# Kernel tuning notes

Measured on AMD Instinct MI355X. Metric: run time of the kernel, lower is better.

Reference implementation:

```python
import jax, jax.numpy as jnp
import numpy as np

N_NODES = 50000
N_EDGES = 800000
NEG_SLOPE = 0.2


def _edge_softmax(scores, dst, n):
    # scores: [E, H]; softmax over edges grouped by destination node
    m = jax.ops.segment_max(scores, dst, num_segments=n)          # [N, H]
    ex = jnp.exp(scores - m[dst])                                 # [E, H]
    s = jax.ops.segment_sum(ex, dst, num_segments=n)              # [N, H]
    return ex / s[dst]


def _gat_layer(h, W, attn_l, attn_r, bias, src, dst, n, heads, out_d):
    feat = (h @ W).reshape(n, heads, out_d)                       # [N, H, D]
    el = jnp.sum(feat * attn_l, axis=-1)                          # [N, H]
    er = jnp.sum(feat * attn_r, axis=-1)                          # [N, H]
    e = jax.nn.leaky_relu(el[src] + er[dst], NEG_SLOPE)           # [E, H]
    alpha = _edge_softmax(e, dst, n)                              # [E, H]
    msg = feat[src] * alpha[:, :, None]                           # [E, H, D]
    rst = jax.ops.segment_sum(msg, dst, num_segments=n)           # [N, H, D]
    return rst + bias.reshape(1, heads, out_d)


def setup_inputs() -> dict:
    key = jax.random.key(0)
    ks = jax.random.split(key, 12)
    in_dim, hid, heads, out_dim = 128, 64, 4, 64
    sc = 0.1
    return {
        "emb": jax.random.normal(ks[0], (N_NODES, in_dim), jnp.float32),
        "src": jax.random.randint(ks[1], (N_EDGES,), 0, N_NODES, jnp.int32),
        "dst": jax.random.randint(ks[2], (N_EDGES,), 0, N_NODES, jnp.int32),
        "W1": jax.random.normal(ks[3], (in_dim, heads * hid), jnp.float32) * sc,
        "attn_l1": jax.random.normal(ks[4], (1, heads, hid), jnp.float32) * sc,
        "attn_r1": jax.random.normal(ks[5], (1, heads, hid), jnp.float32) * sc,
        "b1": jax.random.normal(ks[6], (heads * hid,), jnp.float32) * sc,
        "W2": jax.random.normal(ks[7], (heads * hid, out_dim), jnp.float32) * sc,
        "attn_l2": jax.random.normal(ks[8], (1, 1, out_dim), jnp.float32) * sc,
        "attn_r2": jax.random.normal(ks[9], (1, 1, out_dim), jnp.float32) * sc,
        "b2": jax.random.normal(ks[10], (out_dim,), jnp.float32) * sc,
    }


def reference(emb, src, dst, W1, attn_l1, attn_r1, b1, W2, attn_l2, attn_r2, b2):
    n = emb.shape[0]
    h = _gat_layer(emb, W1, attn_l1, attn_r1, b1, src, dst, n, 4, 64)   # [N,4,64]
    h = jax.nn.relu(h).reshape(n, 4 * 64)                                # [N,256]
    h = _gat_layer(h, W2, attn_l2, attn_r2, b2, src, dst, n, 1, 64)      # [N,1,64]
    return h.reshape(n, 64)
```

## Files before the change

### kernel.cpp

```cpp
#include <hip/hip_runtime.h>
#include <hip/hip_bf16.h>
#include <math.h>

#define DIV_UP(a,b) (((a)+(b)-1)/(b))

typedef __attribute__((ext_vector_type(8))) short short8v;
typedef __attribute__((ext_vector_type(4))) float f32x4;

__device__ __forceinline__ float bf_lo(unsigned u){ union{unsigned x; float f;} v; v.x = u << 16; return v.f; }
__device__ __forceinline__ float bf_hi(unsigned u){ union{unsigned x; float f;} v; v.x = u & 0xffff0000u; return v.f; }
__device__ __forceinline__ unsigned short f2bf(float f){
  union{float f; unsigned u;} v; v.f = f;
  unsigned r = v.u + 0x7fff + ((v.u >> 16) & 1);
  return (unsigned short)(r >> 16);
}
__device__ __forceinline__ unsigned packbf(float a, float b){
  return (unsigned)f2bf(a) | ((unsigned)f2bf(b) << 16);
}
__device__ __forceinline__ float lrelu(float x){ return x > 0.f ? x : 0.2f*x; }

__global__ void k_count_deg(const int* __restrict__ dst, int* __restrict__ deg, int E){
  int i = blockIdx.x*blockDim.x + threadIdx.x;
  if (i < E) atomicAdd(&deg[dst[i]], 1);
}

__global__ __launch_bounds__(256) void k_scan1(const int* __restrict__ deg,
                                               int* __restrict__ blocksum, int N){
  int b = blockIdx.x;
  int base = b*1024 + threadIdx.x*4;
  int s = 0;
  if (base + 3 < N){
    int4 v = *(const int4*)&deg[base];
    s = v.x + v.y + v.z + v.w;
  } else {
    for (int i = 0; i < 4; i++){ int idx = base + i; if (idx < N) s += deg[idx]; }
  }
  #pragma unroll
  for (int o = 32; o; o >>= 1) s += __shfl_down(s, o);
  __shared__ int ws[4];
  int wid = threadIdx.x >> 6, lane = threadIdx.x & 63;
  if (lane == 0) ws[wid] = s;
  __syncthreads();
  if (threadIdx.x == 0) blocksum[b] = ws[0] + ws[1] + ws[2] + ws[3];
}

__global__ void k_scan2(int* __restrict__ blocksum, int nb){
  int lane = threadIdx.x;
  int carry = 0;
  for (int base = 0; base < nb; base += 64){
    int idx = base + lane;
    int orig = (idx < nb) ? blocksum[idx] : 0;
    int v = orig;
    #pragma unroll
    for (int o = 1; o < 64; o <<= 1){ int t = __shfl_up(v, o); if (lane >= o) v += t; }
    if (idx < nb) blocksum[idx] = carry + v - orig;
    carry += __shfl(v, 63);
  }
}

__global__ __launch_bounds__(256) void k_scan3(const int* __restrict__ deg,
                                               const int* __restrict__ blockoff,
                                               int* __restrict__ row_start,
                                               int* __restrict__ cursor, int N){
  int b = blockIdx.x;
  int base = b*1024 + threadIdx.x*4;
  int v[4];
  #pragma unroll
  for (int i = 0; i < 4; i++){ int idx = base + i; v[i] = (idx < N) ? deg[idx] : 0; }
  int s = v[0] + v[1] + v[2] + v[3];
  int lane = threadIdx.x & 63, wid = threadIdx.x >> 6;
  int inc = s;
  #pragma unroll
  for (int o = 1; o < 64; o <<= 1){ int t = __shfl_up(inc, o); if (lane >= o) inc += t; }
  __shared__ int wsum[4];
  if (lane == 63) wsum[wid] = inc;
  __syncthreads();
  int woff = 0;
  #pragma unroll
  for (int i = 0; i < 4; i++) if (i < wid) woff += wsum[i];
  int run = blockoff[b] + woff + inc - s;
  #pragma unroll
  for (int i = 0; i < 4; i++){
    int idx = base + i;
    if (idx < N){ row_start[idx] = run; cursor[idx] = run; run += v[i]; }
  }
  if (base < N && base + 4 >= N) row_start[N] = run;
}

__global__ void k_fillw4(const int* __restrict__ dst, const int* __restrict__ src,
                         int* __restrict__ cursor, int* __restrict__ srcp,
                         int* __restrict__ dstp,
                         const float4* __restrict__ el4, const float4* __restrict__ er4,
                         float4* __restrict__ w4, int E){
  int i = blockIdx.x*blockDim.x + threadIdx.x;
  if (i < E){
    int d = dst[i], s = src[i];
    int p = atomicAdd(&cursor[d], 1);
    srcp[p] = s; dstp[p] = d;
    float4 l = el4[s], r = er4[d];
    float4 w;
    w.x = __expf(lrelu(l.x + r.x));
    w.y = __expf(lrelu(l.y + r.y));
    w.z = __expf(lrelu(l.z + r.z));
    w.w = __expf(lrelu(l.w + r.w));
    w4[p] = w;
  }
}

__global__ void k_edgew1(const int* __restrict__ srcp, const int* __restrict__ dstp,
                         const float* __restrict__ el, const float* __restrict__ er,
                         float* __restrict__ w1, int E){
  int i = blockIdx.x*blockDim.x + threadIdx.x;
  if (i < E) w1[i] = __expf(lrelu(el[srcp[i]] + er[dstp[i]]));
}

template<int K, int H, bool ABF>
__global__ __launch_bounds__(256) void k_gemm_mfma(const void* __restrict__ Av,
      const float* __restrict__ B, int ldb,
      unsigned short* __restrict__ Cbf,
      const float* __restrict__ al, const float* __restrict__ ar,
      float* __restrict__ el, float* __restrict__ er, int M){
  constexpr int KP = K + 8;
  __shared__ alignas(16) __hip_bfloat16 At[64][KP];
  __shared__ alignas(16) __hip_bfloat16 Bt[64][KP];
  __shared__ float elp[2][64], erp[2][64];
  const int tid = threadIdx.x;
  const int lane = tid & 63, w = tid >> 6;
  const int mw = w >> 1, nw = w & 1;
  const int m0 = blockIdx.x * 64, by = blockIdx.y, n0 = by * 64;

  if constexpr (!ABF){
    const float* A = (const float*)Av;
    #pragma unroll
    for (int i = 0; i < K/16; i++){
      int q = tid + i*256;
      int row = q / (K/4), c4 = q % (K/4);
      float4 a = make_float4(0.f,0.f,0.f,0.f);
      if (m0 + row < M) a = *(const float4*)&A[(size_t)(m0+row)*K + c4*4];
      *(uint2*)&At[row][c4*4] = make_uint2(packbf(a.x,a.y), packbf(a.z,a.w));
    }
  } else {
    const __hip_bfloat16* A = (const __hip_bfloat16*)Av;
    #pragma unroll
    for (int i = 0; i < K/32; i++){
      int q = tid + i*256;
      int row = q / (K/8), c8 = q % (K/8);
      uint4 u = make_uint4(0,0,0,0);
      if (m0 + row < M) u = *(const uint4*)&A[(size_t)(m0+row)*K + c8*8];
      *(uint4*)&At[row][c8*8] = u;
    }
  }
  #pragma unroll
  for (int i = 0; i < K/16; i++){
    int q = tid + i*256;
    int c = q & 63, k4 = q >> 6;
    float b0 = B[(size_t)(k4*4+0)*ldb + n0 + c];
    float b1 = B[(size_t)(k4*4+1)*ldb + n0 + c];
    float b2 = B[(size_t)(k4*4+2)*ldb + n0 + c];
    float b3 = B[(size_t)(k4*4+3)*ldb + n0 + c];
    *(uint2*)&Bt[c][k4*4] = make_uint2(packbf(b0,b1), packbf(b2,b3));
  }
  __syncthreads();

  f32x4 acc[2][2];
  #pragma unroll
  for (int i = 0; i < 2; i++)
    #pragma unroll
    for (int j = 0; j < 2; j++)
      #pragma unroll
      for (int r = 0; r < 4; r++) acc[i][j][r] = 0.f;

  const int rbase = mw*32, cbase = nw*32;
  const int fr = lane & 15, fg = lane >> 4;
  #pragma unroll
  for (int ks = 0; ks < K/32; ks++){
    short8v a0 = *(const short8v*)&At[rbase + fr     ][ks*32 + fg*8];
    short8v a1 = *(const short8v*)&At[rbase + 16 + fr][ks*32 + fg*8];
    short8v b0 = *(const short8v*)&Bt[cbase + fr     ][ks*32 + fg*8];
    short8v b1 = *(const short8v*)&Bt[cbase + 16 + fr][ks*32 + fg*8];
    acc[0][0] = __builtin_amdgcn_mfma_f32_16x16x32_bf16(a0, b0, acc[0][0], 0,0,0);
    acc[0][1] = __builtin_amdgcn_mfma_f32_16x16x32_bf16(a0, b1, acc[0][1], 0,0,0);
    acc[1][0] = __builtin_amdgcn_mfma_f32_16x16x32_bf16(a1, b0, acc[1][0], 0,0,0);
    acc[1][1] = __builtin_amdgcn_mfma_f32_16x16x32_bf16(a1, b1, acc[1][1], 0,0,0);
  }

  float alv[2], arv[2];
  #pragma unroll
  for (int nt = 0; nt < 2; nt++){
    int col = cbase + nt*16 + fr;
    alv[nt] = al[by*64 + col];
    arv[nt] = ar[by*64 + col];
  }
  #pragma unroll
  for (int mt = 0; mt < 2; mt++){
    #pragma unroll
    for (int r = 0; r < 4; r++){
      float pl = acc[mt][0][r]*alv[0] + acc[mt][1][r]*alv[1];
      float pr = acc[mt][0][r]*arv[0] + acc[mt][1][r]*arv[1];
      #pragma unroll
      for (int o = 1; o < 16; o <<= 1){ pl += __shfl_xor(pl, o); pr += __shfl_xor(pr, o); }
      if (fr == 0){
        int rl = rbase + mt*16 + fg*4 + r;
        elp[nw][rl] = pl; erp[nw][rl] = pr;
      }
    }
  }
  const int NN = H*64;
  #pragma unroll
  for (int mt = 0; mt < 2; mt++){
    #pragma unroll
    for (int r = 0; r < 4; r++){
      int row = m0 + rbase + mt*16 + fg*4 + r;
      if (row < M){
        #pragma unroll
        for (int nt = 0; nt < 2; nt++)
          Cbf[(size_t)row*NN + n0 + cbase + nt*16 + fr] = f2bf(acc[mt][nt][r]);
      }
    }
  }
  __syncthreads();
  if (tid < 64){
    int row = m0 + tid;
    if (row < M){
      el[(size_t)row*H + by] = elp[0][tid] + elp[1][tid];
      er[(size_t)row*H + by] = erp[0][tid] + erp[1][tid];
    }
  }
}

__global__ __launch_bounds__(256) void k_gath4(const uint4* __restrict__ fbase,
      const float* __restrict__ w4, const int* __restrict__ row_start,
      const int* __restrict__ srcp, const float* __restrict__ bias,
      __hip_bfloat16* __restrict__ outb, int N, int nwaves){
  int wv = threadIdx.x >> 6, lane = threadIdx.x & 63;
  int g = lane >> 4, j = lane & 15, h = j >> 2;
  const unsigned jo2 = (unsigned)(j << 1);

  int n = blockIdx.x*4 + wv;
  if (n >= N) return;
  int rs = row_start[n], re = row_start[n+1];

  while (true){
    int deg = re - rs;
    int nn = n + nwaves;
    int rs_n = 0, re_n = 0;
    if (nn < N){ rs_n = row_start[nn]; re_n = row_start[nn+1]; }

    float acc[16];
    #pragma unroll
    for (int k = 0; k < 16; k++) acc[k] = 0.f;
    float Sacc = 0.f;

    int i = 0;
    int full = deg & ~15;
    for (; i < full; i += 16){
      float wb[4]; uint4 u0[4], u1[4];
      #pragma unroll
      for (int k = 0; k < 4; k++){
        unsigned e = (unsigned)(rs + i + k*4 + g);
        int sb = srcp[e];
        wb[k] = w4[(e << 2) + h];
        unsigned fi = ((unsigned)sb << 5) + jo2;
        u0[k] = fbase[fi];
        u1[k] = fbase[fi + 1];
      }
      #pragma unroll
      for (int k = 0; k < 4; k++){
        float wk = wb[k];
        Sacc += wk;
        acc[0]  += bf_lo(u0[k].x)*wk; acc[1]  += bf_hi(u0[k].x)*wk;
        acc[2]  += bf_lo(u0[k].y)*wk; acc[3]  += bf_hi(u0[k].y)*wk;
        acc[4]  += bf_lo(u0[k].z)*wk; acc[5]  += bf_hi(u0[k].z)*wk;
        acc[6]  += bf_lo(u0[k].w)*wk; acc[7]  += bf_hi(u0[k].w)*wk;
        acc[8]  += bf_lo(u1[k].x)*wk; acc[9]  += bf_hi(u1[k].x)*wk;
        acc[10] += bf_lo(u1[k].y)*wk; acc[11] += bf_hi(u1[k].y)*wk;
        acc[12] += bf_lo(u1[k].z)*wk; acc[13] += bf_hi(u1[k].z)*wk;
        acc[14] += bf_lo(u1[k].w)*wk; acc[15] += bf_hi(u1[k].w)*wk;
      }
    }
    if (i < deg){
      float wb[4]; uint4 u0[4], u1[4];
      #pragma unroll
      for (int k = 0; k < 4; k++){
        int e = i + k*4 + g;
        wb[k] = 0.f;
        u0[k] = make_uint4(0,0,0,0); u1[k] = make_uint4(0,0,0,0);
        if (e < deg){
          unsigned ee = (unsigned)(rs + e);
          int sb = srcp[ee];
          wb[k] = w4[(ee << 2) + h];
          unsigned fi = ((unsigned)sb << 5) + jo2;
          u0[k] = fbase[fi];
          u1[k] = fbase[fi + 1];
        }
      }
      #pragma unroll
      for (int k = 0; k < 4; k++){
        float wk = wb[k];
        Sacc += wk;
        acc[0]  += bf_lo(u0[k].x)*wk; acc[1]  += bf_hi(u0[k].x)*wk;
        acc[2]  += bf_lo(u0[k].y)*wk; acc[3]  += bf_hi(u0[k].y)*wk;
        acc[4]  += bf_lo(u0[k].z)*wk; acc[5]  += bf_hi(u0[k].z)*wk;
        acc[6]  += bf_lo(u0[k].w)*wk; acc[7]  += bf_hi(u0[k].w)*wk;
        acc[8]  += bf_lo(u1[k].x)*wk; acc[9]  += bf_hi(u1[k].x)*wk;
        acc[10] += bf_lo(u1[k].y)*wk; acc[11] += bf_hi(u1[k].y)*wk;
        acc[12] += bf_lo(u1[k].z)*wk; acc[13] += bf_hi(u1[k].z)*wk;
        acc[14] += bf_lo(u1[k].w)*wk; acc[15] += bf_hi(u1[k].w)*wk;
      }
    }

    #pragma unroll
    for (int k = 0; k < 16; k++){
      acc[k] += __shfl_xor(acc[k], 16);
      acc[k] += __shfl_xor(acc[k], 32);
    }
    Sacc += __shfl_xor(Sacc, 16);
    Sacc += __shfl_xor(Sacc, 32);
    if (g == 0){
      float inv = (deg > 0 && Sacc > 0.f) ? 1.f / Sacc : 0.f;
      float4 b0 = *(const float4*)&bias[j*16 + 0];
      float4 b1 = *(const float4*)&bias[j*16 + 4];
      float4 b2 = *(const float4*)&bias[j*16 + 8];
      float4 b3 = *(const float4*)&bias[j*16 + 12];
      float v[16];
      v[0]=acc[0]*inv+b0.x;  v[1]=acc[1]*inv+b0.y;  v[2]=acc[2]*inv+b0.z;  v[3]=acc[3]*inv+b0.w;
      v[4]=acc[4]*inv+b1.x;  v[5]=acc[5]*inv+b1.y;  v[6]=acc[6]*inv+b1.z;  v[7]=acc[7]*inv+b1.w;
      v[8]=acc[8]*inv+b2.x;  v[9]=acc[9]*inv+b2.y;  v[10]=acc[10]*inv+b2.z; v[11]=acc[11]*inv+b2.w;
      v[12]=acc[12]*inv+b3.x; v[13]=acc[13]*inv+b3.y; v[14]=acc[14]*inv+b3.z; v[15]=acc[15]*inv+b3.w;
      #pragma unroll
      for (int k = 0; k < 16; k++) v[k] = fmaxf(v[k], 0.f);
      uint4 o0, o1;
      o0.x = packbf(v[0], v[1]);   o0.y = packbf(v[2], v[3]);
      o0.z = packbf(v[4], v[5]);   o0.w = packbf(v[6], v[7]);
      o1.x = packbf(v[8], v[9]);   o1.y = packbf(v[10], v[11]);
      o1.z = packbf(v[12], v[13]); o1.w = packbf(v[14], v[15]);
      uint4* op = (uint4*)outb + (size_t)n*32 + (j << 1);
      op[0] = o0; op[1] = o1;
    }

    if (nn >= N) break;
    n = nn; rs = rs_n; re = re_n;
  }
}

__global__ __launch_bounds__(256) void k_gath1(const uint2* __restrict__ fbase,
      const float* __restrict__ w1, const int* __restrict__ row_start,
      const int* __restrict__ srcp, const float* __restrict__ bias,
      float* __restrict__ out, int N, int nwaves){
  int wv = threadIdx.x >> 6, lane = threadIdx.x & 63;
  int g = lane >> 4, j = lane & 15;
  const unsigned jo = (unsigned)j;

  int n = blockIdx.x*4 + wv;
  if (n >= N) return;
  int rs = row_start[n], re = row_start[n+1];

  while (true){
    int deg = re - rs;
    int nn = n + nwaves;
    int rs_n = 0, re_n = 0;
    if (nn < N){ rs_n = row_start[nn]; re_n = row_start[nn+1]; }

    float acc[4] = {0.f, 0.f, 0.f, 0.f};
    float Sacc = 0.f;

    int i = 0;
    int full = deg & ~15;
    for (; i < full; i += 16){
      float wb[4]; uint2 u[4];
      #pragma unroll
      for (int k = 0; k < 4; k++){
        unsigned e = (unsigned)(rs + i + k*4 + g);
        int sb = srcp[e];
        wb[k] = w1[e];
        u[k] = fbase[((unsigned)sb << 4) + jo];
      }
      #pragma unroll
      for (int k = 0; k < 4; k++){
        float wk = wb[k];
        Sacc += wk;
        acc[0] += bf_lo(u[k].x)*wk; acc[1] += bf_hi(u[k].x)*wk;
        acc[2] += bf_lo(u[k].y)*wk; acc[3] += bf_hi(u[k].y)*wk;
      }
    }
    if (i < deg){
      float wb[4]; uint2 u[4];
      #pragma unroll
      for (int k = 0; k < 4; k++){
        int e = i + k*4 + g;
        wb[k] = 0.f;
        u[k] = make_uint2(0,0);
        if (e < deg){
          unsigned ee = (unsigned)(rs + e);
          int sb = srcp[ee];
          wb[k] = w1[ee];
          u[k] = fbase[((unsigned)sb << 4) + jo];
        }
      }
      #pragma unroll
      for (int k = 0; k < 4; k++){
        float wk = wb[k];
        Sacc += wk;
        acc[0] += bf_lo(u[k].x)*wk; acc[1] += bf_hi(u[k].x)*wk;
        acc[2] += bf_lo(u[k].y)*wk; acc[3] += bf_hi(u[k].y)*wk;
      }
    }

    #pragma unroll
    for (int k = 0; k < 4; k++){
      acc[k] += __shfl_xor(acc[k], 16);
      acc[k] += __shfl_xor(acc[k], 32);
    }
    Sacc += __shfl_xor(Sacc, 16);
    Sacc += __shfl_xor(Sacc, 32);
    if (g == 0){
      float inv = (deg > 0 && Sacc > 0.f) ? 1.f / Sacc : 0.f;
      float4 b = *(const float4*)&bias[j*4];
      float4 o;
      o.x = acc[0]*inv + b.x; o.y = acc[1]*inv + b.y;
      o.z = acc[2]*inv + b.z; o.w = acc[3]*inv + b.w;
      *(float4*)&out[(size_t)n*64 + j*4] = o;
    }

    if (nn >= N) break;
    n = nn; rs = rs_n; re = re_n;
  }
}

extern "C" void kernel_launch(void* const* d_in, const int* in_sizes, int n_in,
                              void* d_out, int out_size, void* d_ws, size_t ws_size,
                              hipStream_t stream) {
  const float* emb = (const float*)d_in[0];
  const int*   src = (const int*)d_in[1];
  const int*   dst = (const int*)d_in[2];
  const float* W1  = (const float*)d_in[3];
  const float* al1 = (const float*)d_in[4];
  const float* ar1 = (const float*)d_in[5];
  const float* b1  = (const float*)d_in[6];
  const float* W2  = (const float*)d_in[7];
  const float* al2 = (const float*)d_in[8];
  const float* ar2 = (const float*)d_in[9];
  const float* b2  = (const float*)d_in[10];
  float* out = (float*)d_out;

  const int N = in_sizes[0] / 128;
  const int E = in_sizes[1];

  char* p = (char*)d_ws;
  auto alloc = [&](size_t bytes) -> void* {
    void* r = (void*)p; p += (bytes + 255) & ~(size_t)255; return r;
  };
  __hip_bfloat16* feat1b = (__hip_bfloat16*)alloc((size_t)N*256*2);
  __hip_bfloat16* h1b    = (__hip_bfloat16*)alloc((size_t)N*256*2);
  __hip_bfloat16* feat2b = (__hip_bfloat16*)alloc((size_t)N*64*2);
  float* el1             = (float*)alloc((size_t)N*4*4);
  float* er1             = (float*)alloc((size_t)N*4*4);
  float* el2             = (float*)alloc((size_t)N*4);
  float* er2             = (float*)alloc((size_t)N*4);
  int*   deg             = (int*)alloc((size_t)N*4);
  int*   row_start       = (int*)alloc((size_t)(N+1)*4);
  int*   cursor          = (int*)alloc((size_t)N*4);
  int*   blocksum        = (int*)alloc((size_t)DIV_UP(N,1024)*4);
  int*   srcp            = (int*)alloc((size_t)E*4);
  int*   dstp            = (int*)alloc((size_t)E*4);
  float* w4              = (float*)alloc((size_t)E*16);
  float* w1              = w4;

  const int nb = DIV_UP(N, 1024);
  const int gblocks = min(DIV_UP(N, 4), 2048);
  const int nwaves  = gblocks * 4;

  hipMemsetAsync(deg, 0, (size_t)N*4, stream);
  k_count_deg<<<DIV_UP(E,256), 256, 0, stream>>>(dst, deg, E);
  k_scan1<<<nb, 256, 0, stream>>>(deg, blocksum, N);
  k_scan2<<<1, 64, 0, stream>>>(blocksum, nb);
  k_scan3<<<nb, 256, 0, stream>>>(deg, blocksum, row_start, cursor, N);

  k_gemm_mfma<128,4,false><<<dim3(DIV_UP(N,64), 4), 256, 0, stream>>>(
      emb, W1, 256, (unsigned short*)feat1b, al1, ar1, el1, er1, N);
  k_fillw4<<<DIV_UP(E,256), 256, 0, stream>>>(dst, src, cursor, srcp, dstp,
      (const float4*)el1, (const float4*)er1, (float4*)w4, E);
  k_gath4<<<gblocks, 256, 0, stream>>>((const uint4*)feat1b, w4, row_start,
                                       srcp, b1, h1b, N, nwaves);
  k_gemm_mfma<256,1,true><<<dim3(DIV_UP(N,64), 1), 256, 0, stream>>>(
      h1b, W2, 64, (unsigned short*)feat2b, al2, ar2, el2, er2, N);
  k_edgew1<<<DIV_UP(E,256), 256, 0, stream>>>(srcp, dstp, el2, er2, w1, E);
  k_gath1<<<gblocks, 256, 0, stream>>>((const uint2*)feat2b, w1, row_start,
                                       srcp, b2, out, N, nwaves);
}
```

Measured before the change: 235.4 us.

## Fold block-offset scan into scan3 and loop GEMM1 over heads per block

Removes the single-wave k_scan2 launch: each scan3 block now computes its own block offset by summing the preceding block sums inside one wave. The layer-1 GEMM becomes a dedicated kernel where each block loads and converts its 64-row A tile to bf16 once and loops over all four 64-column head tiles, instead of a 2D grid that reloads A per head. This cuts one launch and the repeated A traffic and bf16 conversion, at the cost of fewer blocks and serialized B-tile loads inside each block.

Measured after the change: 229.3 us. -2.6%, faster.

```diff
diff --git a/kernel.cpp b/kernel.cpp
--- a/kernel.cpp
+++ b/kernel.cpp
@@ -44,25 +44,22 @@
   if (threadIdx.x == 0) blocksum[b] = ws[0] + ws[1] + ws[2] + ws[3];
 }
 
-__global__ void k_scan2(int* __restrict__ blocksum, int nb){
-  int lane = threadIdx.x;
-  int carry = 0;
-  for (int base = 0; base < nb; base += 64){
-    int idx = base + lane;
-    int orig = (idx < nb) ? blocksum[idx] : 0;
-    int v = orig;
-    #pragma unroll
-    for (int o = 1; o < 64; o <<= 1){ int t = __shfl_up(v, o); if (lane >= o) v += t; }
-    if (idx < nb) blocksum[idx] = carry + v - orig;
-    carry += __shfl(v, 63);
-  }
-}
-
 __global__ __launch_bounds__(256) void k_scan3(const int* __restrict__ deg,
-                                               const int* __restrict__ blockoff,
+                                               const int* __restrict__ blocksum, int nb,
                                                int* __restrict__ row_start,
                                                int* __restrict__ cursor, int N){
   int b = blockIdx.x;
+  __shared__ int s_boff;
+  if (threadIdx.x < 64){
+    int acc = 0;
+    for (int base = 0; base < nb; base += 64){
+      int idx = base + threadIdx.x;
+      if (idx < nb && idx < b) acc += blocksum[idx];
+    }
+    #pragma unroll
+    for (int o = 32; o; o >>= 1) acc += __shfl_down(acc, o);
+    if (threadIdx.x == 0) s_boff = acc;
+  }
   int base = b*1024 + threadIdx.x*4;
   int v[4];
   #pragma unroll
@@ -78,7 +75,7 @@
   int woff = 0;
   #pragma unroll
   for (int i = 0; i < 4; i++) if (i < wid) woff += wsum[i];
-  int run = blockoff[b] + woff + inc - s;
+  int run = s_boff + woff + inc - s;
   #pragma unroll
   for (int i = 0; i < 4; i++){
     int idx = base + i;
@@ -112,6 +109,109 @@
                          float* __restrict__ w1, int E){
   int i = blockIdx.x*blockDim.x + threadIdx.x;
   if (i < E) w1[i] = __expf(lrelu(el[srcp[i]] + er[dstp[i]]));
+}
+
+__global__ __launch_bounds__(256) void k_gemm1loop(const float* __restrict__ A,
+      const float* __restrict__ B,
+      unsigned short* __restrict__ Cbf,
+      const float* __restrict__ al, const float* __restrict__ ar,
+      float* __restrict__ el, float* __restrict__ er, int M){
+  __shared__ alignas(16) __hip_bfloat16 At[64][136];
+  __shared__ alignas(16) __hip_bfloat16 Bt[64][136];
+  __shared__ float elp[2][64], erp[2][64];
+  const int tid = threadIdx.x;
+  const int lane = tid & 63, w = tid >> 6;
+  const int mw = w >> 1, nw = w & 1;
+  const int m0 = blockIdx.x * 64;
+  const int rbase = mw*32, cbase = nw*32;
+  const int fr = lane & 15, fg = lane >> 4;
+
+  #pragma unroll
+  for (int i = 0; i < 8; i++){
+    int q = tid + i*256;
+    int row = q >> 5, c4 = q & 31;
+    float4 a = make_float4(0.f,0.f,0.f,0.f);
+    if (m0 + row < M) a = *(const float4*)&A[(size_t)(m0+row)*128 + c4*4];
+    *(uint2*)&At[row][c4*4] = make_uint2(packbf(a.x,a.y), packbf(a.z,a.w));
+  }
+
+  for (int by = 0; by < 4; by++){
+    int n0 = by * 64;
+    __syncthreads();
+    #pragma unroll
+    for (int i = 0; i < 8; i++){
+      int q = tid + i*256;
+      int c = q & 63, k4 = q >> 6;
+      float b0 = B[(size_t)(k4*4+0)*256 + n0 + c];
+      float b1 = B[(size_t)(k4*4+1)*256 + n0 + c];
+      float b2 = B[(size_t)(k4*4+2)*256 + n0 + c];
+      float b3 = B[(size_t)(k4*4+3)*256 + n0 + c];
+      *(uint2*)&Bt[c][k4*4] = make_uint2(packbf(b0,b1), packbf(b2,b3));
+    }
+    __syncthreads();
+
+    f32x4 acc[2][2];
+    #pragma unroll
+    for (int i = 0; i < 2; i++)
+      #pragma unroll
+      for (int jj = 0; jj < 2; jj++)
+        #pragma unroll
+        for (int r = 0; r < 4; r++) acc[i][jj][r] = 0.f;
+
+    #pragma unroll
+    for (int ks = 0; ks < 4; ks++){
+      short8v a0 = *(const short8v*)&At[rbase + fr     ][ks*32 + fg*8];
+      short8v a1 = *(const short8v*)&At[rbase + 16 + fr][ks*32 + fg*8];
+      short8v b0 = *(const short8v*)&Bt[cbase + fr     ][ks*32 + fg*8];
+      short8v b1 = *(const short8v*)&Bt[cbase + 16 + fr][ks*32 + fg*8];
+      acc[0][0] = __builtin_amdgcn_mfma_f32_16x16x32_bf16(a0, b0, acc[0][0], 0,0,0);
+      acc[0][1] = __builtin_amdgcn_mfma_f32_16x16x32_bf16(a0, b1, acc[0][1], 0,0,0);
+      acc[1][0] = __builtin_amdgcn_mfma_f32_16x16x32_bf16(a1, b0, acc[1][0], 0,0,0);
+      acc[1][1] = __builtin_amdgcn_mfma_f32_16x16x32_bf16(a1, b1, acc[1][1], 0,0,0);
+    }
+
+    float alv[2], arv[2];
+    #pragma unroll
+    for (int nt = 0; nt < 2; nt++){
+      int col = cbase + nt*16 + fr;
+      alv[nt] = al[n0 + col];
+      arv[nt] = ar[n0 + col];
+    }
+    #pragma unroll
+    for (int mt = 0; mt < 2; mt++){
+      #pragma unroll
+      for (int r = 0; r < 4; r++){
+        float pl = acc[mt][0][r]*alv[0] + acc[mt][1][r]*alv[1];
+        float pr = acc[mt][0][r]*arv[0] + acc[mt][1][r]*arv[1];
+        #pragma unroll
+        for (int o = 1; o < 16; o <<= 1){ pl += __shfl_xor(pl, o); pr += __shfl_xor(pr, o); }
+        if (fr == 0){
+          int rl = rbase + mt*16 + fg*4 + r;
+          elp[nw][rl] = pl; erp[nw][rl] = pr;
+        }
+      }
+    }
+    #pragma unroll
+    for (int mt = 0; mt < 2; mt++){
+      #pragma unroll
+      for (int r = 0; r < 4; r++){
+        int row = m0 + rbase + mt*16 + fg*4 + r;
+        if (row < M){
+          #pragma unroll
+          for (int nt = 0; nt < 2; nt++)
+            Cbf[(size_t)row*256 + n0 + cbase + nt*16 + fr] = f2bf(acc[mt][nt][r]);
+        }
+      }
+    }
+    __syncthreads();
+    if (tid < 64){
+      int row = m0 + tid;
+      if (row < M){
+        el[(size_t)row*4 + by] = elp[0][tid] + elp[1][tid];
+        er[(size_t)row*4 + by] = erp[0][tid] + erp[1][tid];
+      }
+    }
+  }
 }
 
 template<int K, int H, bool ABF>
@@ -473,11 +573,10 @@
   hipMemsetAsync(deg, 0, (size_t)N*4, stream);
   k_count_deg<<<DIV_UP(E,256), 256, 0, stream>>>(dst, deg, E);
   k_scan1<<<nb, 256, 0, stream>>>(deg, blocksum, N);
-  k_scan2<<<1, 64, 0, stream>>>(blocksum, nb);
-  k_scan3<<<nb, 256, 0, stream>>>(deg, blocksum, row_start, cursor, N);
-
-  k_gemm_mfma<128,4,false><<<dim3(DIV_UP(N,64), 4), 256, 0, stream>>>(
-      emb, W1, 256, (unsigned short*)feat1b, al1, ar1, el1, er1, N);
+  k_scan3<<<nb, 256, 0, stream>>>(deg, blocksum, nb, row_start, cursor, N);
+
+  k_gemm1loop<<<DIV_UP(N,64), 256, 0, stream>>>(emb, W1, (unsigned short*)feat1b,
+                                                al1, ar1, el1, er1, N);
   k_fillw4<<<DIV_UP(E,256), 256, 0, stream>>>(dst, src, cursor, srcp, dstp,
       (const float4*)el1, (const float4*)er1, (float4*)w4, E);
   k_gath4<<<gblocks, 256, 0, stream>>>((const uint4*)feat1b, w4, row_start,
```
